# Optimization experiments

Hardware: AMD Instinct MI355X
Metric: run time of the kernel (lower is better)

## Reference

```python
import jax, jax.numpy as jnp
import numpy as np

N_NODES = 50000   # total nodes across the batch of graphs
N_EDGES = 800000  # avg degree 16
F_IN = 128        # num_features
DIM = 256         # hidden dim
N_LAYERS = 3      # num_gc_layers
N_GRAPHS = 512    # graphs in the batch (max(batch)+1)
BN_EPS = 1e-5


def setup_inputs() -> dict:
    key = jax.random.key(0)
    ks = jax.random.split(key, 16)
    inp = {}
    inp["x"] = jax.random.normal(ks[0], (N_NODES, F_IN), dtype=jnp.float32)
    inp["edge_index"] = jax.random.randint(ks[1], (2, N_EDGES), 0, N_NODES, dtype=jnp.int64)
    inp["batch"] = jnp.sort(jax.random.randint(ks[2], (N_NODES,), 0, N_GRAPHS, dtype=jnp.int64))
    k = 3
    for i in range(N_LAYERS):
        fin = F_IN if i == 0 else DIM
        inp[f"w1_{i}"] = jax.random.normal(ks[k], (fin, DIM), dtype=jnp.float32) / np.sqrt(fin); k += 1
        inp[f"b1_{i}"] = jnp.zeros((DIM,), dtype=jnp.float32)
        inp[f"w2_{i}"] = jax.random.normal(ks[k], (DIM, DIM), dtype=jnp.float32) / np.sqrt(DIM); k += 1
        inp[f"b2_{i}"] = jnp.zeros((DIM,), dtype=jnp.float32)
        inp[f"bn_g{i}"] = jnp.ones((DIM,), dtype=jnp.float32)
        inp[f"bn_b{i}"] = jnp.zeros((DIM,), dtype=jnp.float32)
    return inp


def _gin_layer(h, src, dst, w1, b1, w2, b2, g, b):
    # GINConv (eps=0): agg_i = h_i + sum_{j->i} h_j  (scatter-add over edges)
    agg = h + jax.ops.segment_sum(h[src], dst, num_segments=N_NODES)
    # MLP: Linear -> ReLU -> Linear
    m = jnp.maximum(agg @ w1 + b1, 0.0) @ w2 + b2
    # F.relu then BatchNorm1d (training mode: batch statistics, biased var)
    m = jnp.maximum(m, 0.0)
    mu = m.mean(axis=0)
    var = ((m - mu) ** 2).mean(axis=0)
    return g * (m - mu) / jnp.sqrt(var + BN_EPS) + b


def reference(x, edge_index, batch,
              w1_0, b1_0, w2_0, b2_0, bn_g0, bn_b0,
              w1_1, b1_1, w2_1, b2_1, bn_g1, bn_b1,
              w1_2, b1_2, w2_2, b2_2, bn_g2, bn_b2):
    src, dst = edge_index[0], edge_index[1]
    params = [
        (w1_0, b1_0, w2_0, b2_0, bn_g0, bn_b0),
        (w1_1, b1_1, w2_1, b2_1, bn_g1, bn_b1),
        (w1_2, b1_2, w2_2, b2_2, bn_g2, bn_b2),
    ]
    xs = []
    h = x
    for p in params:
        h = _gin_layer(h, src, dst, *p)
        xs.append(h)
    # global add-pool readout per layer, concat along feature dim
    pooled = jnp.concatenate(
        [jax.ops.segment_sum(hi, batch, num_segments=N_GRAPHS) for hi in xs], axis=1)
    return pooled, jnp.concatenate(xs, axis=1)
```

## Files before the change

kernel.cpp:

```cpp
#include <hip/hip_runtime.h>

#define N_NODES 50000
#define N_EDGES 800000
#define F_IN 128
#define DIM 256
#define N_GRAPHS 512
#define BN_EPS 1e-5f

typedef unsigned short u16;
typedef unsigned int u32;
using floatx4 = __attribute__((ext_vector_type(4))) float;
using short8 = __attribute__((ext_vector_type(8))) short;
using half2v = __attribute__((ext_vector_type(2))) _Float16;

#if __has_builtin(__builtin_amdgcn_fdot2)
#define HAS_FDOT2 1
#endif

__device__ __forceinline__ u16 f2h(float f) {
    _Float16 h = (_Float16)f;
    return __builtin_bit_cast(u16, h);
}
__device__ __forceinline__ float hlo(u32 u) {
    half2v h = __builtin_bit_cast(half2v, u);
    return (float)h.x;
}
__device__ __forceinline__ float hhi(u32 u) {
    half2v h = __builtin_bit_cast(half2v, u);
    return (float)h.y;
}
__device__ __forceinline__ u32 pack2(float a, float b) {
    half2v h = {(_Float16)a, (_Float16)b};
    return __builtin_bit_cast(u32, h);
}
__device__ __forceinline__ void dacc(u32 w, float& a, float& b) {
#ifdef HAS_FDOT2
    half2v v = __builtin_bit_cast(half2v, w);
    const half2v L = {(_Float16)1.0f, (_Float16)0.0f};
    const half2v Hm = {(_Float16)0.0f, (_Float16)1.0f};
    a = __builtin_amdgcn_fdot2(v, L, a, false);
    b = __builtin_amdgcn_fdot2(v, Hm, b, false);
#else
    a += hlo(w);
    b += hhi(w);
#endif
}
__device__ __forceinline__ void load_lds16(const void* g, void* l) {
    __builtin_amdgcn_global_load_lds((const __attribute__((address_space(1))) void*)g,
                                     (__attribute__((address_space(3))) void*)l, 16, 0, 0);
}


__global__ void count_deg(const int* __restrict__ dst, int* __restrict__ deg, int nE) {
    int e = blockIdx.x * 256 + threadIdx.x;
    if (e < nE) atomicAdd(&deg[dst[e]], 1);
}

__global__ void scan_block(const int* __restrict__ deg, int* __restrict__ row_start,
                           int* __restrict__ bsum, int n) {
    __shared__ int wtot[4];
    int i = blockIdx.x * 256 + threadIdx.x;
    int lane = threadIdx.x & 63, w = threadIdx.x >> 6;
    int v = (i < n) ? deg[i] : 0;
    int s = v;
#pragma unroll
    for (int d = 1; d < 64; d <<= 1) {
        int t = __shfl_up(s, d);
        if (lane >= d) s += t;
    }
    if (lane == 63) wtot[w] = s;
    __syncthreads();
    int off = 0;
#pragma unroll
    for (int k = 0; k < 4; ++k)
        if (k < w) off += wtot[k];
    s += off;
    if (i < n) row_start[i + 1] = s;
    if (threadIdx.x == 255) bsum[blockIdx.x] = s;
}

__global__ void scan_partials(const int* __restrict__ bsum, int* __restrict__ boff,
                              int* __restrict__ row_start, int* __restrict__ cursor, int nb) {
    __shared__ int wtot[4];
    int i = threadIdx.x;
    int lane = i & 63, w = i >> 6;
    int v = (i < nb) ? bsum[i] : 0;
    int s = v;
#pragma unroll
    for (int d = 1; d < 64; d <<= 1) {
        int t = __shfl_up(s, d);
        if (lane >= d) s += t;
    }
    if (lane == 63) wtot[w] = s;
    __syncthreads();
    int off = 0;
#pragma unroll
    for (int k = 0; k < 4; ++k)
        if (k < w) off += wtot[k];
    boff[i] = s + off - v;
    if (i == 0) { row_start[0] = 0; cursor[0] = 0; }
}

__global__ void add_offsets(int* __restrict__ row_start, int* __restrict__ cursor,
                            const int* __restrict__ boff, int n) {
    int i = blockIdx.x * 256 + threadIdx.x;
    if (i < n) {
        int fin = row_start[i + 1] + boff[blockIdx.x];
        row_start[i + 1] = fin;
        cursor[i + 1] = fin;
    }
}

__global__ void fill_csr(const int* __restrict__ src, const int* __restrict__ dst,
                         int* __restrict__ cursor, int* __restrict__ srcs, int nE) {
    int e = blockIdx.x * 256 + threadIdx.x;
    if (e < nE) {
        int p = atomicAdd(&cursor[dst[e]], 1);
        srcs[p] = src[e];
    }
}


__global__ void convert_all(const float4* __restrict__ x4, uint2* __restrict__ Hout, int n4,
                            const float* __restrict__ w10, const float* __restrict__ w11,
                            const float* __restrict__ w12, const float* __restrict__ w20,
                            const float* __restrict__ w21, const float* __restrict__ w22,
                            u16* __restrict__ Wall) {
    int i = blockIdx.x * 256 + threadIdx.x;
    if (i < n4) {
        float4 v = x4[i];
        uint2 p;
        p.x = pack2(v.x, v.y);
        p.y = pack2(v.z, v.w);
        Hout[i] = p;
        return;
    }
    int j = i - n4;
    if (j >= 360448) return;
    const float* w;
    int K, base;
    if (j < 32768)       { w = w10; K = 128; base = 0; }
    else if (j < 98304)  { w = w11; K = 256; base = 32768; }
    else if (j < 163840) { w = w12; K = 256; base = 98304; }
    else if (j < 229376) { w = w20; K = 256; base = 163840; }
    else if (j < 294912) { w = w21; K = 256; base = 229376; }
    else                 { w = w22; K = 256; base = 294912; }
    int loc = j - base;
    int nn = loc / K, kk = loc - nn * K;
    Wall[j] = f2h(w[(size_t)kk * 256 + nn]);
}


template <int K, int AFFINE>
__global__ __launch_bounds__(256) void aggregate_v2(
    const u16* __restrict__ h, const int* __restrict__ row_start,
    const int* __restrict__ srcs, u16* __restrict__ outp,
    const float* __restrict__ sums, const float* __restrict__ g,
    const float* __restrict__ bb, float inv_n, int n) {
    constexpr int RW = K / 2;
    constexpr int NSUB = (K == 256) ? 2 : 4;
    int node = (int)(((size_t)blockIdx.x * blockDim.x + threadIdx.x) >> 6);
    int lane = threadIdx.x & 63;
    if (node >= n) return;
    const u32* hb = (const u32*)h;
    const int sub = lane / (64 / NSUB);
    const int li = lane % (64 / NSUB);

    float acc[8];
#pragma unroll
    for (int t = 0; t < 8; ++t) acc[t] = 0.f;
    {
        if (sub == 0) {
            uint4 v = *(const uint4*)(hb + (size_t)node * RW + li * 4);
            dacc(v.x, acc[0], acc[1]);
            dacc(v.y, acc[2], acc[3]);
            dacc(v.z, acc[4], acc[5]);
            dacc(v.w, acc[6], acc[7]);
        }
    }

    int s = row_start[node], e = row_start[node + 1];
    for (int j0 = s; j0 < e; j0 += 64) {
        int myidx = (j0 + lane < e) ? srcs[j0 + lane] : 0;
        int cnt = min(64, e - j0);
        int j = 0;
        for (; j + NSUB * 8 - 1 < cnt; j += NSUB * 8) {
            uint4 gg[8];
#pragma unroll
            for (int q = 0; q < 8; ++q) {
                int sq = __shfl(myidx, j + q * NSUB + sub);
                gg[q] = *(const uint4*)(hb + (size_t)sq * RW + li * 4);
            }
#pragma unroll
            for (int q = 0; q < 8; ++q) {
                dacc(gg[q].x, acc[0], acc[1]);
                dacc(gg[q].y, acc[2], acc[3]);
                dacc(gg[q].z, acc[4], acc[5]);
                dacc(gg[q].w, acc[6], acc[7]);
            }
        }
        for (; j + NSUB * 4 - 1 < cnt; j += NSUB * 4) {
            uint4 gg[4];
#pragma unroll
            for (int q = 0; q < 4; ++q) {
                int sq = __shfl(myidx, j + q * NSUB + sub);
                gg[q] = *(const uint4*)(hb + (size_t)sq * RW + li * 4);
            }
#pragma unroll
            for (int q = 0; q < 4; ++q) {
                dacc(gg[q].x, acc[0], acc[1]);
                dacc(gg[q].y, acc[2], acc[3]);
                dacc(gg[q].z, acc[4], acc[5]);
                dacc(gg[q].w, acc[6], acc[7]);
            }
        }
        for (; j < cnt; j += NSUB) {
            int idx = j + sub;
            bool valid = idx < cnt;
            int sq = __shfl(myidx, valid ? idx : j);
            if (valid) {
                uint4 gg = *(const uint4*)(hb + (size_t)sq * RW + li * 4);
                dacc(gg.x, acc[0], acc[1]);
                dacc(gg.y, acc[2], acc[3]);
                dacc(gg.z, acc[4], acc[5]);
                dacc(gg.w, acc[6], acc[7]);
            }
        }
    }

    if (NSUB == 4) {
#pragma unroll
        for (int t = 0; t < 8; ++t) acc[t] += __shfl_xor(acc[t], 16);
    }
#pragma unroll
    for (int t = 0; t < 8; ++t) acc[t] += __shfl_xor(acc[t], 32);

    if (sub == 0) {
        if (AFFINE) {
            int c = li * 8;
            float degp1 = (float)(e - s + 1);
            float4 s1a = *(const float4*)(sums + c), s1b = *(const float4*)(sums + c + 4);
            float4 s2a = *(const float4*)(sums + 256 + c), s2b = *(const float4*)(sums + 256 + c + 4);
            float4 g4a = *(const float4*)(g + c), g4b = *(const float4*)(g + c + 4);
            float4 b4a = *(const float4*)(bb + c), b4b = *(const float4*)(bb + c + 4);
            float mu[8] = {s1a.x, s1a.y, s1a.z, s1a.w, s1b.x, s1b.y, s1b.z, s1b.w};
            float q2[8] = {s2a.x, s2a.y, s2a.z, s2a.w, s2b.x, s2b.y, s2b.z, s2b.w};
            float gv[8] = {g4a.x, g4a.y, g4a.z, g4a.w, g4b.x, g4b.y, g4b.z, g4b.w};
            float bv[8] = {b4a.x, b4a.y, b4a.z, b4a.w, b4b.x, b4b.y, b4b.z, b4b.w};
#pragma unroll
            for (int t = 0; t < 8; ++t) {
                float m = mu[t] * inv_n;
                float sc = gv[t] / sqrtf(q2[t] * inv_n - m * m + BN_EPS);
                float sh = bv[t] - m * sc;
                acc[t] = sc * acc[t] + degp1 * sh;
            }
        }
        uint4 o;
        o.x = pack2(acc[0], acc[1]);
        o.y = pack2(acc[2], acc[3]);
        o.z = pack2(acc[4], acc[5]);
        o.w = pack2(acc[6], acc[7]);
        *(uint4*)((u32*)outp + (size_t)node * RW + li * 4) = o;
    }
}


template <int K1>
__global__ __launch_bounds__(512, 2) void mlp_fused(
    const u16* __restrict__ A, const u16* __restrict__ B1t, const float* __restrict__ b1,
    const u16* __restrict__ B2t, const float* __restrict__ b2,
    u16* __restrict__ Cout, float* __restrict__ sums, int M) {
    __shared__ u16 As[64 * 64];
    __shared__ u16 Bs[256 * 64];
    __shared__ u16 Ts[64 * 256];
    const int tid = threadIdx.x;
    const int w = tid >> 6, lane = tid & 63;
    const int wm = w >> 2, wn = w & 3;
    const int r = lane & 15, rg = lane >> 4;
    const int bm = blockIdx.x * 64;

    floatx4 acc[2][4];
#pragma unroll
    for (int i = 0; i < 2; ++i)
#pragma unroll
        for (int j = 0; j < 4; ++j) acc[i][j] = (floatx4){0.f, 0.f, 0.f, 0.f};

    for (int k0 = 0; k0 < K1; k0 += 64) {
        __syncthreads();
        {
            int arow = bm + (tid >> 3);
            if (arow >= M) arow = M - 1;
            int swz = (tid & 7) ^ ((tid >> 3) & 7);
            load_lds16(A + (size_t)arow * K1 + k0 + swz * 8, As + w * 512);
        }
#pragma unroll
        for (int q = 0; q < 4; ++q) {
            int i = q * 512 + tid;
            int nrow = i >> 3;
            int swz = (i & 7) ^ (nrow & 7);
            load_lds16(B1t + (size_t)nrow * K1 + k0 + swz * 8, Bs + q * 4096 + w * 512);
        }
        __syncthreads();
        short8 a[2][2], b[4][2];
#pragma unroll
        for (int mi = 0; mi < 2; ++mi) {
            int row = wm * 32 + mi * 16 + r;
#pragma unroll
            for (int kk = 0; kk < 2; ++kk) {
                int ck = (kk * 4 + rg) ^ (row & 7);
                a[mi][kk] = *(const short8*)(As + row * 64 + ck * 8);
            }
        }
#pragma unroll
        for (int ni = 0; ni < 4; ++ni) {
            int row = wn * 64 + ni * 16 + r;
#pragma unroll
            for (int kk = 0; kk < 2; ++kk) {
                int ck = (kk * 4 + rg) ^ (row & 7);
                b[ni][kk] = *(const short8*)(Bs + row * 64 + ck * 8);
            }
        }
#pragma unroll
        for (int kk = 0; kk < 2; ++kk)
#pragma unroll
            for (int mi = 0; mi < 2; ++mi)
#pragma unroll
                for (int ni = 0; ni < 4; ++ni)
                    acc[mi][ni] = __builtin_amdgcn_mfma_f32_16x16x32_f16(a[mi][kk], b[ni][kk], acc[mi][ni], 0, 0, 0);
    }
#pragma unroll
    for (int ni = 0; ni < 4; ++ni) {
        int col = wn * 64 + ni * 16 + r;
        float bv = b1[col];
#pragma unroll
        for (int mi = 0; mi < 2; ++mi)
#pragma unroll
            for (int rr = 0; rr < 4; ++rr) {
                int lrow = wm * 32 + mi * 16 + rg * 4 + rr;
                float v = fmaxf(acc[mi][ni][rr] + bv, 0.f);
                int chunk = (col >> 3) ^ (lrow & 7);
                *(u16*)((char*)Ts + lrow * 512 + chunk * 16 + (col & 7) * 2) = f2h(v);
            }
#pragma unroll
        for (int mi = 0; mi < 2; ++mi) acc[mi][ni] = (floatx4){0.f, 0.f, 0.f, 0.f};
    }

    for (int k0 = 0; k0 < 256; k0 += 64) {
        __syncthreads();
#pragma unroll
        for (int q = 0; q < 4; ++q) {
            int i = q * 512 + tid;
            int nrow = i >> 3;
            int swz = (i & 7) ^ (nrow & 7);
            load_lds16(B2t + (size_t)nrow * 256 + k0 + swz * 8, Bs + q * 4096 + w * 512);
        }
        __syncthreads();
        short8 a[2][2], b[4][2];
#pragma unroll
        for (int mi = 0; mi < 2; ++mi) {
            int lrow = wm * 32 + mi * 16 + r;
#pragma unroll
            for (int kk = 0; kk < 2; ++kk) {
                int ck = ((k0 >> 3) + kk * 4 + rg) ^ (lrow & 7);
                a[mi][kk] = *(const short8*)((const char*)Ts + lrow * 512 + ck * 16);
            }
        }
#pragma unroll
        for (int ni = 0; ni < 4; ++ni) {
            int row = wn * 64 + ni * 16 + r;
#pragma unroll
            for (int kk = 0; kk < 2; ++kk) {
                int ck = (kk * 4 + rg) ^ (row & 7);
                b[ni][kk] = *(const short8*)(Bs + row * 64 + ck * 8);
            }
        }
#pragma unroll
        for (int kk = 0; kk < 2; ++kk)
#pragma unroll
            for (int mi = 0; mi < 2; ++mi)
#pragma unroll
                for (int ni = 0; ni < 4; ++ni)
                    acc[mi][ni] = __builtin_amdgcn_mfma_f32_16x16x32_f16(a[mi][kk], b[ni][kk], acc[mi][ni], 0, 0, 0);
    }

#pragma unroll
    for (int ni = 0; ni < 4; ++ni) {
        int col = wn * 64 + ni * 16 + r;
        float bv = b2[col];
        float s = 0.f, s2 = 0.f;
#pragma unroll
        for (int mi = 0; mi < 2; ++mi)
#pragma unroll
            for (int rr = 0; rr < 4; ++rr) {
                int row = bm + wm * 32 + mi * 16 + rg * 4 + rr;
                if (row < M) {
                    float v = fmaxf(acc[mi][ni][rr] + bv, 0.f);
                    u16 qb = f2h(v);
                    float vq = hlo((u32)qb);
                    Cout[(size_t)row * 256 + col] = qb;
                    s += vq;
                    s2 += vq * vq;
                }
            }
        s += __shfl_xor(s, 16);
        s += __shfl_xor(s, 32);
        s2 += __shfl_xor(s2, 16);
        s2 += __shfl_xor(s2, 32);
        if (rg == 0) {
            atomicAdd(&sums[col], s);
            atomicAdd(&sums[256 + col], s2);
        }
    }
}


__global__ void bn_pool(const u16* __restrict__ Mb, const float* __restrict__ sums,
                        const float* __restrict__ g, const float* __restrict__ bb,
                        const int* __restrict__ batch, float* __restrict__ out_nodes,
                        float* __restrict__ pooled, int col_off, int n, float inv_n) {
    int w = threadIdx.x >> 6, lane = threadIdx.x & 63;
    int base = blockIdx.x * 64 + w * 16;
    if (base >= n) return;
    int c4 = lane << 2;
    float4 s1 = *(const float4*)(sums + c4);
    float4 s2 = *(const float4*)(sums + 256 + c4);
    float4 g4 = *(const float4*)(g + c4);
    float4 b4 = *(const float4*)(bb + c4);
    float4 sc, sh;
    {
        float mux = s1.x * inv_n, muy = s1.y * inv_n, muz = s1.z * inv_n, muw = s1.w * inv_n;
        sc.x = g4.x / sqrtf(s2.x * inv_n - mux * mux + BN_EPS);
        sc.y = g4.y / sqrtf(s2.y * inv_n - muy * muy + BN_EPS);
        sc.z = g4.z / sqrtf(s2.z * inv_n - muz * muz + BN_EPS);
        sc.w = g4.w / sqrtf(s2.w * inv_n - muw * muw + BN_EPS);
        sh.x = b4.x - mux * sc.x;
        sh.y = b4.y - muy * sc.y;
        sh.z = b4.z - muz * sc.z;
        sh.w = b4.w - muw * sc.w;
    }
    float4 acc = make_float4(0.f, 0.f, 0.f, 0.f);
    int gcur = -1;
    int end = min(base + 16, n);
    for (int row = base; row < end; ++row) {
        uint2 pk = *(const uint2*)(Mb + (size_t)row * 256 + c4);
        float4 o;
        o.x = fmaf(hlo(pk.x), sc.x, sh.x);
        o.y = fmaf(hhi(pk.x), sc.y, sh.y);
        o.z = fmaf(hlo(pk.y), sc.z, sh.z);
        o.w = fmaf(hhi(pk.y), sc.w, sh.w);
        floatx4 ov = {o.x, o.y, o.z, o.w};
        __builtin_nontemporal_store(ov, (floatx4*)(out_nodes + (size_t)row * 768 + col_off + c4));
        int gg = batch[row];
        if (gg != gcur) {
            if (gcur >= 0) {
                float* pp = pooled + (size_t)gcur * 768 + col_off + c4;
                atomicAdd(pp + 0, acc.x);
                atomicAdd(pp + 1, acc.y);
                atomicAdd(pp + 2, acc.z);
                atomicAdd(pp + 3, acc.w);
            }
            gcur = gg;
            acc = o;
        } else {
            acc.x += o.x; acc.y += o.y; acc.z += o.z; acc.w += o.w;
        }
    }
    if (gcur >= 0) {
        float* pp = pooled + (size_t)gcur * 768 + col_off + c4;
        atomicAdd(pp + 0, acc.x);
        atomicAdd(pp + 1, acc.y);
        atomicAdd(pp + 2, acc.z);
        atomicAdd(pp + 3, acc.w);
    }
}


extern "C" void kernel_launch(void* const* d_in, const int* in_sizes, int n_in,
                              void* d_out, int out_size, void* d_ws, size_t ws_size,
                              hipStream_t stream) {
    const float* x = (const float*)d_in[0];
    const int* esrc = (const int*)d_in[1];
    const int* edst = esrc + N_EDGES;
    const int* batch = (const int*)d_in[2];

    const float* w1[3] = {(const float*)d_in[3], (const float*)d_in[9], (const float*)d_in[15]};
    const float* b1[3] = {(const float*)d_in[4], (const float*)d_in[10], (const float*)d_in[16]};
    const float* w2[3] = {(const float*)d_in[5], (const float*)d_in[11], (const float*)d_in[17]};
    const float* b2[3] = {(const float*)d_in[6], (const float*)d_in[12], (const float*)d_in[18]};
    const float* bng[3] = {(const float*)d_in[7], (const float*)d_in[13], (const float*)d_in[19]};
    const float* bnb[3] = {(const float*)d_in[8], (const float*)d_in[14], (const float*)d_in[20]};

    float* out_pooled = (float*)d_out;
    float* out_nodes = (float*)d_out + (size_t)N_GRAPHS * 768;

    char* p = (char*)d_ws;
    u16* Abf = (u16*)p; p += (size_t)N_NODES * 256 * 2;
    u16* Mb = (u16*)p;  p += (size_t)N_NODES * 256 * 2;
    u16* H = (u16*)p;   p += (size_t)N_NODES * 256 * 2;
    u16* Wall = (u16*)p; p += (size_t)360448 * 2;
    float* sums = (float*)p; p += 3 * 512 * 4;
    int* deg = (int*)p;      p += (size_t)N_NODES * 4;
    const size_t zero_bytes = 3 * 512 * 4 + (size_t)N_NODES * 4;
    int* row_start = (int*)p; p += (size_t)(N_NODES + 1) * 4;
    int* cursor = (int*)p;    p += (size_t)(N_NODES + 1) * 4;
    int* srcs = (int*)p;      p += (size_t)N_EDGES * 4;
    int* bsum = (int*)p;      p += 256 * 4;
    int* boff = (int*)p;      p += 256 * 4;

    const u16* W1t[3] = {Wall, Wall + 32768, Wall + 98304};
    const u16* W2t[3] = {Wall + 163840, Wall + 229376, Wall + 294912};

    const int NBLK = (N_NODES + 255) / 256;

    hipMemsetAsync(sums, 0, zero_bytes, stream);
    hipMemsetAsync(out_pooled, 0, (size_t)N_GRAPHS * 768 * sizeof(float), stream);

    count_deg<<<(N_EDGES + 255) / 256, 256, 0, stream>>>(edst, deg, N_EDGES);
    scan_block<<<NBLK, 256, 0, stream>>>(deg, row_start, bsum, N_NODES);
    scan_partials<<<1, 256, 0, stream>>>(bsum, boff, row_start, cursor, NBLK);
    add_offsets<<<NBLK, 256, 0, stream>>>(row_start, cursor, boff, N_NODES);
    fill_csr<<<(N_EDGES + 255) / 256, 256, 0, stream>>>(esrc, edst, cursor, srcs, N_EDGES);

    {
        const int n4 = N_NODES * F_IN / 4;
        const int tot = n4 + 360448;
        convert_all<<<(tot + 255) / 256, 256, 0, stream>>>(
            (const float4*)x, (uint2*)H, n4,
            w1[0], w1[1], w1[2], w2[0], w2[1], w2[2], Wall);
    }

    const int AGRID = (N_NODES + 3) / 4;
    const int MGRID = (N_NODES + 63) / 64;
    const int PBLK = (N_NODES + 63) / 64;
    const float inv_n = 1.0f / N_NODES;

    aggregate_v2<128, 0><<<AGRID, 256, 0, stream>>>(H, row_start, srcs, Abf,
                                                    nullptr, nullptr, nullptr, inv_n, N_NODES);
    mlp_fused<128><<<MGRID, 512, 0, stream>>>(Abf, W1t[0], b1[0], W2t[0], b2[0], Mb, sums, N_NODES);
    aggregate_v2<256, 1><<<AGRID, 256, 0, stream>>>(Mb, row_start, srcs, Abf,
                                                    sums, bng[0], bnb[0], inv_n, N_NODES);
    bn_pool<<<PBLK, 256, 0, stream>>>(Mb, sums, bng[0], bnb[0], batch, out_nodes, out_pooled,
                                      0, N_NODES, inv_n);
    mlp_fused<256><<<MGRID, 512, 0, stream>>>(Abf, W1t[1], b1[1], W2t[1], b2[1], Mb, sums + 512, N_NODES);
    aggregate_v2<256, 1><<<AGRID, 256, 0, stream>>>(Mb, row_start, srcs, Abf,
                                                    sums + 512, bng[1], bnb[1], inv_n, N_NODES);
    bn_pool<<<PBLK, 256, 0, stream>>>(Mb, sums + 512, bng[1], bnb[1], batch, out_nodes, out_pooled,
                                      256, N_NODES, inv_n);
    mlp_fused<256><<<MGRID, 512, 0, stream>>>(Abf, W1t[2], b1[2], W2t[2], b2[2], Mb, sums + 1024, N_NODES);
    bn_pool<<<PBLK, 256, 0, stream>>>(Mb, sums + 1024, bng[2], bnb[2], batch, out_nodes, out_pooled,
                                      512, N_NODES, inv_n);
}
```

Before: 695.8 us.

## Co-schedule BN+pool of previous layer inside next layer's MLP kernel launch

After: 653.4 us. -6.1%, faster.

```diff
diff --git a/kernel.cpp b/kernel.cpp
--- a/kernel.cpp
+++ b/kernel.cpp
@@ -266,18 +266,80 @@
 
 
 template <int K1>
-__global__ __launch_bounds__(512, 2) void mlp_fused(
+__global__ __launch_bounds__(512, 2) void mlp_bn(
     const u16* __restrict__ A, const u16* __restrict__ B1t, const float* __restrict__ b1,
     const u16* __restrict__ B2t, const float* __restrict__ b2,
-    u16* __restrict__ Cout, float* __restrict__ sums, int M) {
+    u16* __restrict__ Cout, float* __restrict__ sums_out, int M, int nBn,
+    const u16* __restrict__ Mprev, const float* __restrict__ sums_in,
+    const float* __restrict__ g, const float* __restrict__ bb,
+    const int* __restrict__ batch, float* __restrict__ out_nodes,
+    float* __restrict__ pooled, int col_off, float inv_n) {
     __shared__ u16 As[64 * 64];
     __shared__ u16 Bs[256 * 64];
     __shared__ u16 Ts[64 * 256];
     const int tid = threadIdx.x;
     const int w = tid >> 6, lane = tid & 63;
+
+    if ((int)blockIdx.x < nBn) {
+        int base = blockIdx.x * 128 + w * 16;
+        if (base >= M) return;
+        int c4 = lane << 2;
+        float4 s1 = *(const float4*)(sums_in + c4);
+        float4 s2 = *(const float4*)(sums_in + 256 + c4);
+        float4 g4 = *(const float4*)(g + c4);
+        float4 b4 = *(const float4*)(bb + c4);
+        float4 sc, sh;
+        {
+            float mux = s1.x * inv_n, muy = s1.y * inv_n, muz = s1.z * inv_n, muw = s1.w * inv_n;
+            sc.x = g4.x / sqrtf(s2.x * inv_n - mux * mux + BN_EPS);
+            sc.y = g4.y / sqrtf(s2.y * inv_n - muy * muy + BN_EPS);
+            sc.z = g4.z / sqrtf(s2.z * inv_n - muz * muz + BN_EPS);
+            sc.w = g4.w / sqrtf(s2.w * inv_n - muw * muw + BN_EPS);
+            sh.x = b4.x - mux * sc.x;
+            sh.y = b4.y - muy * sc.y;
+            sh.z = b4.z - muz * sc.z;
+            sh.w = b4.w - muw * sc.w;
+        }
+        float4 acc = make_float4(0.f, 0.f, 0.f, 0.f);
+        int gcur = -1;
+        int end = min(base + 16, M);
+        for (int row = base; row < end; ++row) {
+            uint2 pk = *(const uint2*)(Mprev + (size_t)row * 256 + c4);
+            float4 o;
+            o.x = fmaf(hlo(pk.x), sc.x, sh.x);
+            o.y = fmaf(hhi(pk.x), sc.y, sh.y);
+            o.z = fmaf(hlo(pk.y), sc.z, sh.z);
+            o.w = fmaf(hhi(pk.y), sc.w, sh.w);
+            floatx4 ov = {o.x, o.y, o.z, o.w};
+            __builtin_nontemporal_store(ov, (floatx4*)(out_nodes + (size_t)row * 768 + col_off + c4));
+            int gg = batch[row];
+            if (gg != gcur) {
+                if (gcur >= 0) {
+                    float* pp = pooled + (size_t)gcur * 768 + col_off + c4;
+                    atomicAdd(pp + 0, acc.x);
+                    atomicAdd(pp + 1, acc.y);
+                    atomicAdd(pp + 2, acc.z);
+                    atomicAdd(pp + 3, acc.w);
+                }
+                gcur = gg;
+                acc = o;
+            } else {
+                acc.x += o.x; acc.y += o.y; acc.z += o.z; acc.w += o.w;
+            }
+        }
+        if (gcur >= 0) {
+            float* pp = pooled + (size_t)gcur * 768 + col_off + c4;
+            atomicAdd(pp + 0, acc.x);
+            atomicAdd(pp + 1, acc.y);
+            atomicAdd(pp + 2, acc.z);
+            atomicAdd(pp + 3, acc.w);
+        }
+        return;
+    }
+
     const int wm = w >> 2, wn = w & 3;
     const int r = lane & 15, rg = lane >> 4;
-    const int bm = blockIdx.x * 64;
+    const int bm = (blockIdx.x - nBn) * 64;
 
     floatx4 acc[2][4];
 #pragma unroll
@@ -407,8 +469,8 @@
         s2 += __shfl_xor(s2, 16);
         s2 += __shfl_xor(s2, 32);
         if (rg == 0) {
-            atomicAdd(&sums[col], s);
-            atomicAdd(&sums[256 + col], s2);
+            atomicAdd(&sums_out[col], s);
+            atomicAdd(&sums_out[256 + col], s2);
         }
     }
 }
@@ -495,7 +557,8 @@
 
     char* p = (char*)d_ws;
     u16* Abf = (u16*)p; p += (size_t)N_NODES * 256 * 2;
-    u16* Mb = (u16*)p;  p += (size_t)N_NODES * 256 * 2;
+    u16* Mb0 = (u16*)p; p += (size_t)N_NODES * 256 * 2;
+    u16* Mb1 = (u16*)p; p += (size_t)N_NODES * 256 * 2;
     u16* H = (u16*)p;   p += (size_t)N_NODES * 256 * 2;
     u16* Wall = (u16*)p; p += (size_t)360448 * 2;
     float* sums = (float*)p; p += 3 * 512 * 4;
@@ -531,22 +594,28 @@
 
     const int AGRID = (N_NODES + 3) / 4;
     const int MGRID = (N_NODES + 63) / 64;
+    const int BGRID = (N_NODES + 127) / 128;
     const int PBLK = (N_NODES + 63) / 64;
     const float inv_n = 1.0f / N_NODES;
 
     aggregate_v2<128, 0><<<AGRID, 256, 0, stream>>>(H, row_start, srcs, Abf,
                                                     nullptr, nullptr, nullptr, inv_n, N_NODES);
-    mlp_fused<128><<<MGRID, 512, 0, stream>>>(Abf, W1t[0], b1[0], W2t[0], b2[0], Mb, sums, N_NODES);
-    aggregate_v2<256, 1><<<AGRID, 256, 0, stream>>>(Mb, row_start, srcs, Abf,
+    mlp_bn<128><<<MGRID, 512, 0, stream>>>(Abf, W1t[0], b1[0], W2t[0], b2[0], Mb0, sums,
+                                           N_NODES, 0,
+                                           nullptr, nullptr, nullptr, nullptr,
+                                           nullptr, nullptr, nullptr, 0, inv_n);
+    aggregate_v2<256, 1><<<AGRID, 256, 0, stream>>>(Mb0, row_start, srcs, Abf,
                                                     sums, bng[0], bnb[0], inv_n, N_NODES);
-    bn_pool<<<PBLK, 256, 0, stream>>>(Mb, sums, bng[0], bnb[0], batch, out_nodes, out_pooled,
-                                      0, N_NODES, inv_n);
-    mlp_fused<256><<<MGRID, 512, 0, stream>>>(Abf, W1t[1], b1[1], W2t[1], b2[1], Mb, sums + 512, N_NODES);
-    aggregate_v2<256, 1><<<AGRID, 256, 0, stream>>>(Mb, row_start, srcs, Abf,
+    mlp_bn<256><<<BGRID + MGRID, 512, 0, stream>>>(Abf, W1t[1], b1[1], W2t[1], b2[1], Mb1, sums + 512,
+                                                   N_NODES, BGRID,
+                                                   Mb0, sums, bng[0], bnb[0],
+                                                   batch, out_nodes, out_pooled, 0, inv_n);
+    aggregate_v2<256, 1><<<AGRID, 256, 0, stream>>>(Mb1, row_start, srcs, Abf,
                                                     sums + 512, bng[1], bnb[1], inv_n, N_NODES);
-    bn_pool<<<PBLK, 256, 0, stream>>>(Mb, sums + 512, bng[1], bnb[1], batch, out_nodes, out_pooled,
-                                      256, N_NODES, inv_n);
-    mlp_fused<256><<<MGRID, 512, 0, stream>>>(Abf, W1t[2], b1[2], W2t[2], b2[2], Mb, sums + 1024, N_NODES);
-    bn_pool<<<PBLK, 256, 0, stream>>>(Mb, sums + 1024, bng[2], bnb[2], batch, out_nodes, out_pooled,
+    mlp_bn<256><<<BGRID + MGRID, 512, 0, stream>>>(Abf, W1t[2], b1[2], W2t[2], b2[2], Mb0, sums + 1024,
+                                                   N_NODES, BGRID,
+                                                   Mb1, sums + 512, bng[1], bnb[1],
+                                                   batch, out_nodes, out_pooled, 256, inv_n);
+    bn_pool<<<PBLK, 256, 0, stream>>>(Mb0, sums + 1024, bng[2], bnb[2], batch, out_nodes, out_pooled,
                                       512, N_NODES, inv_n);
 }
```
